# Kernel optimization log

Hardware: AMD Instinct MI355X
Metric: run time of the kernel (lower is better)

## Reference

```python
import jax, jax.numpy as jnp
import numpy as np

N_HEADS = 12
D_MODEL = 768
D_HEAD = 64
LN_EPS = 1e-5


def setup_inputs() -> dict:
    key = jax.random.key(0)
    ks = jax.random.split(key, 7)
    bs, slen = 1, 4096
    s_in = 1.0 / np.sqrt(D_MODEL)
    s_out = 1.0 / np.sqrt(N_HEADS * D_HEAD)
    return {
        "x": jax.random.normal(ks[0], (bs, slen, D_MODEL), jnp.float32),
        "W_attn": jax.random.uniform(ks[1], (D_MODEL, 3 * N_HEADS * D_HEAD), jnp.float32, -s_in, s_in),
        "b_attn": jax.random.uniform(ks[2], (3 * N_HEADS * D_HEAD,), jnp.float32, -s_in, s_in),
        "W_out": jax.random.uniform(ks[3], (N_HEADS * D_HEAD, D_MODEL), jnp.float32, -s_out, s_out),
        "b_out": jax.random.uniform(ks[4], (D_MODEL,), jnp.float32, -s_out, s_out),
        "ln_g": jnp.ones((D_MODEL,), jnp.float32),
        "ln_b": jnp.zeros((D_MODEL,), jnp.float32),
    }


def reference(x, W_attn, b_attn, W_out, b_out, ln_g, ln_b):
    bs, slen, _ = x.shape
    qkv = x @ W_attn + b_attn                      # [b, s, 3*H*D]
    wq, wk, wv = jnp.split(qkv, 3, axis=-1)
    def to_heads(t):
        return t.reshape(bs, slen, N_HEADS, D_HEAD)
    q, k, v = to_heads(wq), to_heads(wk), to_heads(wv)
    # scores: [b, h, s_q, s_k]
    scores = jnp.einsum('bqhd,bkhd->bhqk', q, k) / np.sqrt(D_HEAD).astype(np.float32)
    probs = jax.nn.softmax(scores, axis=-1)
    attn = jnp.einsum('bhqk,bkhd->bqhd', probs, v).reshape(bs, slen, N_HEADS * D_HEAD)
    out = attn @ W_out + b_out
    y = x + out
    mu = jnp.mean(y, axis=-1, keepdims=True)
    var = jnp.mean(jnp.square(y - mu), axis=-1, keepdims=True)
    return (y - mu) / jnp.sqrt(var + LN_EPS) * ln_g + ln_b
```

## Files before the change

### kernel.cpp

```cpp
#include <hip/hip_runtime.h>
#include <cstdint>
#include <cstddef>

#define SL 4096
#define DM 768

typedef short s16x8 __attribute__((ext_vector_type(8)));
typedef unsigned short u16x8 __attribute__((ext_vector_type(8)));
typedef unsigned short u16x4 __attribute__((ext_vector_type(4)));
typedef float f32x4 __attribute__((ext_vector_type(4)));
typedef float f32x16 __attribute__((ext_vector_type(16)));
typedef unsigned int u32x4 __attribute__((ext_vector_type(4)));

__device__ __forceinline__ unsigned short f2bf(float f) {
  unsigned u = __float_as_uint(f);
  u = u + 0x7fffu + ((u >> 16) & 1u);
  return (unsigned short)(u >> 16);
}

__device__ __forceinline__ int swz(int row, int col) {
  return (row << 6) + ((((col >> 3) ^ row) & 7) << 3) + (col & 7);
}

#define ASYNC16(G, L)                                                        \
  __builtin_amdgcn_global_load_lds(                                          \
      (const __attribute__((address_space(1))) void*)(G),                    \
      (__attribute__((address_space(3))) void*)(L), 16, 0, 0)

#define WAITB()                                   \
  do {                                            \
    asm volatile("s_waitcnt vmcnt(0)" ::: "memory"); \
    __builtin_amdgcn_s_barrier();                 \
  } while (0)

#define MF32(A, B, C) __builtin_amdgcn_mfma_f32_32x32x16_bf16((A), (B), (C), 0, 0, 0)

__device__ __forceinline__ void tr_body(
    const float* __restrict__ in, unsigned short* __restrict__ out,
    int R, int C, int bx, int by, float (*tile)[65], int t) {
  const int r0 = by * 64, c0 = bx * 64;
  const int lr = t >> 2, lcb = (t & 3) * 16;
  #pragma unroll
  for (int j = 0; j < 16; j += 4) {
    f32x4 v = *reinterpret_cast<const f32x4*>(in + (size_t)(r0 + lr) * C + c0 + lcb + j);
    tile[lr][lcb + j + 0] = v[0];
    tile[lr][lcb + j + 1] = v[1];
    tile[lr][lcb + j + 2] = v[2];
    tile[lr][lcb + j + 3] = v[3];
  }
  __syncthreads();
  #pragma unroll
  for (int j = 0; j < 16; j += 4) {
    u16x4 o;
    o[0] = f2bf(tile[lcb + j + 0][lr]);
    o[1] = f2bf(tile[lcb + j + 1][lr]);
    o[2] = f2bf(tile[lcb + j + 2][lr]);
    o[3] = f2bf(tile[lcb + j + 3][lr]);
    *reinterpret_cast<u16x4*>(out + (size_t)(c0 + lr) * R + r0 + lcb + j) = o;
  }
}

extern "C" __global__ __launch_bounds__(256) void k_prep(
    const float* __restrict__ x, const float* __restrict__ Wa,
    const float* __restrict__ Wo, unsigned short* __restrict__ xbf,
    unsigned short* __restrict__ wat, unsigned short* __restrict__ wot,
    unsigned* __restrict__ kmx) {
  __shared__ float tile[64][65];
  const int b = blockIdx.x, t = threadIdx.x;
  if (b < 3072) {
    if (b == 0 && t < 12) kmx[t] = 0u;
    const int i = (b * 256 + t) * 4;
    f32x4 v = *reinterpret_cast<const f32x4*>(x + i);
    u16x4 o;
    o[0] = f2bf(v[0]); o[1] = f2bf(v[1]); o[2] = f2bf(v[2]); o[3] = f2bf(v[3]);
    *reinterpret_cast<u16x4*>(xbf + i) = o;
  } else if (b < 3504) {
    const int bb = b - 3072;
    tr_body(Wa, wat, 768, 2304, bb % 36, bb / 36, tile, t);
  } else {
    const int bb = b - 3504;
    tr_body(Wo, wot, 768, 768, bb % 12, bb / 12, tile, t);
  }
}

extern "C" __global__ __launch_bounds__(256) void k_qkv(
    const unsigned short* __restrict__ xbf, const unsigned short* __restrict__ wt,
    const float* __restrict__ bias, unsigned short* __restrict__ qb,
    unsigned short* __restrict__ kbo, unsigned short* __restrict__ vtb,
    float* __restrict__ qn2, unsigned* __restrict__ kmx) {
  __shared__ alignas(16) unsigned short a_lds[2][8192];
  __shared__ alignas(16) unsigned short b_lds[2][8192];
  const int t = threadIdx.x, w = t >> 6, l = t & 63;
  const int l15 = l & 15, lg = l >> 4;
  const int wr = w >> 1, wc = w & 1;
  const int n0 = blockIdx.x * 128, m0 = blockIdx.y * 128;
  f32x4 acc[4][4];
  #pragma unroll
  for (int mt = 0; mt < 4; mt++)
    #pragma unroll
    for (int nt = 0; nt < 4; nt++) acc[mt][nt] = (f32x4)0.f;
  int soff[4];
  #pragma unroll
  for (int c = 0; c < 4; c++) {
    int i = c * 256 + t;
    int row = i >> 3, bp = i & 7;
    soff[c] = row * DM + (bp ^ (row & 7)) * 8;
  }
  const unsigned short* asrc = xbf + (size_t)m0 * DM;
  const unsigned short* bsrc = wt + (size_t)n0 * DM;

#define STAGE128(B, KK)                                                   \
  do {                                                                    \
    _Pragma("unroll")                                                     \
    for (int c = 0; c < 4; c++) {                                         \
      ASYNC16(asrc + (KK) + soff[c], &a_lds[B][0] + c * 2048 + w * 512);  \
      ASYNC16(bsrc + (KK) + soff[c], &b_lds[B][0] + c * 2048 + w * 512);  \
    }                                                                     \
  } while (0)

#define GEMM128(B)                                                            \
  do {                                                                        \
    _Pragma("unroll")                                                         \
    for (int kc = 0; kc < 2; kc++) {                                          \
      s16x8 af[4], bfv[4];                                                    \
      _Pragma("unroll")                                                       \
      for (int mt = 0; mt < 4; mt++)                                          \
        af[mt] = *reinterpret_cast<const s16x8*>(                             \
            &a_lds[B][swz(wr * 64 + mt * 16 + l15, kc * 32 + lg * 8)]);       \
      _Pragma("unroll")                                                       \
      for (int nt = 0; nt < 4; nt++)                                          \
        bfv[nt] = *reinterpret_cast<const s16x8*>(                            \
            &b_lds[B][swz(wc * 64 + nt * 16 + l15, kc * 32 + lg * 8)]);       \
      _Pragma("unroll")                                                       \
      for (int mt = 0; mt < 4; mt++)                                          \
        _Pragma("unroll")                                                     \
        for (int nt = 0; nt < 4; nt++)                                        \
          acc[mt][nt] = __builtin_amdgcn_mfma_f32_16x16x32_bf16(              \
              af[mt], bfv[nt], acc[mt][nt], 0, 0, 0);                         \
    }                                                                         \
  } while (0)

  STAGE128(0, 0);
  WAITB();
  #pragma unroll 1
  for (int kk = 0; kk < DM; kk += 128) {
    STAGE128(1, kk + 64);
    GEMM128(0);
    WAITB();
    if (kk + 128 < DM) STAGE128(0, kk + 128);
    GEMM128(1);
    WAITB();
  }
#undef STAGE128
#undef GEMM128

  const int secn = (n0 >= 1536) ? 2 : (n0 >= 768 ? 1 : 0);
  const int nbase = n0 - secn * 768 + wc * 64;
  const int h = nbase >> 6;
  const int mrow0 = m0 + wr * 64;
  float bv4[4];
  #pragma unroll
  for (int nt = 0; nt < 4; nt++) bv4[nt] = bias[secn * 768 + nbase + nt * 16 + l15];

  if (secn == 0) {
    const float QS = 0.180336880f;
    float s2[4][4];
    #pragma unroll
    for (int mt = 0; mt < 4; mt++) {
      #pragma unroll
      for (int r = 0; r < 4; r++) s2[mt][r] = 0.f;
    }
    #pragma unroll
    for (int mt = 0; mt < 4; mt++) {
      #pragma unroll
      for (int nt = 0; nt < 4; nt++) {
        const int d = nt * 16 + l15;
        #pragma unroll
        for (int r = 0; r < 4; r++) {
          const int m = mrow0 + mt * 16 + lg * 4 + r;
          float v = (acc[mt][nt][r] + bv4[nt]) * QS;
          qb[((size_t)h * SL + m) * 64 + d] = f2bf(v);
          s2[mt][r] = fmaf(v, v, s2[mt][r]);
        }
      }
    }
    #pragma unroll
    for (int mt = 0; mt < 4; mt++)
      #pragma unroll
      for (int r = 0; r < 4; r++) {
        #pragma unroll
        for (int off = 1; off < 16; off <<= 1)
          s2[mt][r] += __shfl_xor(s2[mt][r], off, 64);
      }
    if (l15 == 0) {
      #pragma unroll
      for (int mt = 0; mt < 4; mt++)
        #pragma unroll
        for (int r = 0; r < 4; r++)
          qn2[(size_t)h * SL + mrow0 + mt * 16 + lg * 4 + r] = s2[mt][r];
    }
  } else if (secn == 1) {
    float s2[4][4];
    #pragma unroll
    for (int mt = 0; mt < 4; mt++) {
      #pragma unroll
      for (int r = 0; r < 4; r++) s2[mt][r] = 0.f;
    }
    #pragma unroll
    for (int mt = 0; mt < 4; mt++) {
      #pragma unroll
      for (int nt = 0; nt < 4; nt++) {
        const int d = nt * 16 + l15;
        #pragma unroll
        for (int r = 0; r < 4; r++) {
          const int m = mrow0 + mt * 16 + lg * 4 + r;
          float v = acc[mt][nt][r] + bv4[nt];
          kbo[((size_t)h * SL + m) * 64 + d] = f2bf(v);
          s2[mt][r] = fmaf(v, v, s2[mt][r]);
        }
      }
    }
    float rm = 0.f;
    #pragma unroll
    for (int mt = 0; mt < 4; mt++)
      #pragma unroll
      for (int r = 0; r < 4; r++) {
        #pragma unroll
        for (int off = 1; off < 16; off <<= 1)
          s2[mt][r] += __shfl_xor(s2[mt][r], off, 64);
        rm = fmaxf(rm, s2[mt][r]);
      }
    rm = fmaxf(rm, __shfl_xor(rm, 16, 64));
    rm = fmaxf(rm, __shfl_xor(rm, 32, 64));
    if (l == 0) atomicMax(kmx + h, __float_as_uint(rm));
  } else {
    #pragma unroll
    for (int mt = 0; mt < 4; mt++) {
      #pragma unroll
      for (int nt = 0; nt < 4; nt++) {
        const int d = nt * 16 + l15;
        u16x4 o;
        #pragma unroll
        for (int r = 0; r < 4; r++) o[r] = f2bf(acc[mt][nt][r] + bv4[nt]);
        *reinterpret_cast<u16x4*>(
            vtb + ((size_t)h * 64 + d) * SL + mrow0 + mt * 16 + lg * 4) = o;
      }
    }
  }
}

__device__ __forceinline__ void attn_body32f(
    const unsigned short* kb, const unsigned short* vb,
    const s16x8* qf, f32x16* ot, f32x16& lacc, s16x8 qm,
    const int* kfo, const int* vfo, s16x8 ones) {
  f32x16 st = (f32x16)0.f;
  __builtin_amdgcn_s_setprio(1);
  #pragma unroll
  for (int c = 0; c < 4; c++) {
    s16x8 kf = *reinterpret_cast<const s16x8*>(&kb[kfo[c]]);
    st = MF32(kf, qf[c], st);
  }
  st = MF32(ones, qm, st);
  __builtin_amdgcn_s_setprio(0);
  #pragma unroll
  for (int r = 0; r < 16; r++) st[r] = exp2f(st[r]);
  #pragma unroll
  for (int m = 0; m < 2; m++) {
    const int m0 = m * 8;
    unsigned w0, w1, w2, w3;
    asm("v_cvt_pk_bf16_f32 %0, %1, %2" : "=v"(w0) : "v"(st[m0 + 0]), "v"(st[m0 + 1]));
    asm("v_cvt_pk_bf16_f32 %0, %1, %2" : "=v"(w1) : "v"(st[m0 + 2]), "v"(st[m0 + 3]));
    asm("v_cvt_pk_bf16_f32 %0, %1, %2" : "=v"(w2) : "v"(st[m0 + 4]), "v"(st[m0 + 5]));
    asm("v_cvt_pk_bf16_f32 %0, %1, %2" : "=v"(w3) : "v"(st[m0 + 6]), "v"(st[m0 + 7]));
    asm volatile("v_permlane32_swap_b32 %0, %1" : "+v"(w0), "+v"(w2));
    asm volatile("v_permlane32_swap_b32 %0, %1" : "+v"(w1), "+v"(w3));
    u32x4 wv_;
    wv_[0] = w0; wv_[1] = w1; wv_[2] = w2; wv_[3] = w3;
    s16x8 pbf = *reinterpret_cast<s16x8*>(&wv_);
    __builtin_amdgcn_s_setprio(1);
    #pragma unroll
    for (int dt = 0; dt < 2; dt++) {
      s16x8 vf = *reinterpret_cast<const s16x8*>(&vb[vfo[m * 2 + dt]]);
      ot[dt] = MF32(vf, pbf, ot[dt]);
    }
    lacc = MF32(ones, pbf, lacc);
    __builtin_amdgcn_s_setprio(0);
  }
}

extern "C" __global__ __launch_bounds__(256) void k_attn(
    const unsigned short* __restrict__ qb, const unsigned short* __restrict__ kbi,
    const unsigned short* __restrict__ vt, const float* __restrict__ qn2,
    const unsigned* __restrict__ kmx, unsigned short* __restrict__ aout) {
  __shared__ alignas(16) unsigned char smem[32768];
  unsigned short* kst = (unsigned short*)smem;
  unsigned short* vst = (unsigned short*)(smem + 16384);
  const int t = threadIdx.x, w = t >> 6, l = t & 63;
  const int l31 = l & 31, s = l >> 5;
  const int half = w >> 1, qs = w & 1;
  const int bid = blockIdx.x;
  const int sid = (bid & 7) * 96 + (bid >> 3);
  const int h = sid >> 6, qt = sid & 63;
  const unsigned short* qh = qb + (size_t)h * SL * 64;
  const unsigned short* kh = kbi + ((size_t)h * SL + half * 2048) * 64;
  const unsigned short* vh = vt + (size_t)h * 64 * SL + half * 2048;
  const int q = qt * 64 + qs * 32 + l31;
  const float M = sqrtf(qn2[(size_t)h * SL + q] * __uint_as_float(kmx[h]));
  s16x8 qf[4];
  #pragma unroll
  for (int c = 0; c < 4; c++)
    qf[c] = *reinterpret_cast<const s16x8*>(qh + (size_t)q * 64 + c * 16 + s * 8);
  s16x8 ones;
  #pragma unroll
  for (int e = 0; e < 8; e++) ones[e] = (short)0x3F80;
  s16x8 qm = (s16x8)0;
  if (s == 0) qm[0] = (short)f2bf(-M);
  f32x16 ot[2];
  ot[0] = (f32x16)0.f;
  ot[1] = (f32x16)0.f;
  f32x16 lacc = (f32x16)0.f;
  int koff[2], voff[2];
  #pragma unroll
  for (int c = 0; c < 2; c++) {
    int i = (qs * 2 + c) * 64 + l;
    int row = i >> 3, sb = i & 7;
    int bp = sb ^ ((row ^ (row >> 3)) & 7);
    koff[c] = row * 64 + bp * 8;
    int d = row + 32 * (bp >> 2);
    voff[c] = d * SL + (bp & 3) * 8;
  }
  const int sr = (l31 ^ (l31 >> 3)) & 7;
  int kfo[4], vfo[4];
  #pragma unroll
  for (int c = 0; c < 4; c++) kfo[c] = (l31 << 6) + (((c * 2 + s) ^ sr) << 3);
  #pragma unroll
  for (int m = 0; m < 2; m++)
    #pragma unroll
    for (int dt = 0; dt < 2; dt++)
      vfo[m * 2 + dt] = (l31 << 6) + (((dt * 4 + m * 2 + s) ^ sr) << 3);

#define STAGE_KV(B, LB)                                                     \
  do {                                                                      \
    _Pragma("unroll")                                                       \
    for (int c = 0; c < 2; c++) {                                           \
      ASYNC16(kh + (size_t)(LB) * 64 + koff[c],                             \
              kst + (half * 2 + (B)) * 2048 + (qs * 2 + c) * 512);          \
      ASYNC16(vh + (LB) + voff[c],                                          \
              vst + (half * 2 + (B)) * 2048 + (qs * 2 + c) * 512);          \
    }                                                                       \
  } while (0)

  STAGE_KV(0, 0);
  #pragma unroll 1
  for (int lb = 0; lb < 2048; lb += 64) {
    STAGE_KV(1, lb + 32);
    asm volatile("s_waitcnt vmcnt(4)" ::: "memory");
    __builtin_amdgcn_s_barrier();
    attn_body32f(kst + (half * 2) * 2048, vst + (half * 2) * 2048,
                 qf, ot, lacc, qm, kfo, vfo, ones);
    if (lb + 64 < 2048) {
      STAGE_KV(0, lb + 64);
      asm volatile("s_waitcnt vmcnt(4)" ::: "memory");
    } else {
      asm volatile("s_waitcnt vmcnt(0)" ::: "memory");
    }
    __builtin_amdgcn_s_barrier();
    attn_body32f(kst + (half * 2 + 1) * 2048, vst + (half * 2 + 1) * 2048,
                 qf, ot, lacc, qm, kfo, vfo, ones);
  }
#undef STAGE_KV
  const float lsum = lacc[0];
  float* o_m = (float*)smem;
  float* l_m = (float*)(smem + 17408);
  __syncthreads();
  if (half == 1) {
    #pragma unroll
    for (int dt = 0; dt < 2; dt++) {
      #pragma unroll
      for (int rq = 0; rq < 4; rq++) {
        f32x4 v;
        #pragma unroll
        for (int j = 0; j < 4; j++) v[j] = ot[dt][rq * 4 + j];
        *reinterpret_cast<f32x4*>(&o_m[(qs * 32 + l31) * 68 + dt * 32 + rq * 8 + s * 4]) = v;
      }
    }
    if (s == 0) l_m[qs * 32 + l31] = lsum;
  }
  __syncthreads();
  if (half == 0) {
    const float linv = 1.f / (lsum + l_m[qs * 32 + l31]);
    #pragma unroll
    for (int dt = 0; dt < 2; dt++) {
      #pragma unroll
      for (int rq = 0; rq < 4; rq++) {
        f32x4 vb_ = *reinterpret_cast<const f32x4*>(&o_m[(qs * 32 + l31) * 68 + dt * 32 + rq * 8 + s * 4]);
        u16x4 o;
        #pragma unroll
        for (int j = 0; j < 4; j++)
          o[j] = f2bf((ot[dt][rq * 4 + j] + vb_[j]) * linv);
        *reinterpret_cast<u16x4*>(aout + (size_t)q * DM + h * 64 + dt * 32 + rq * 8 + s * 4) = o;
      }
    }
  }
}

extern "C" __global__ __launch_bounds__(256) void k_out(
    const unsigned short* __restrict__ abf, const unsigned short* __restrict__ wot,
    const float* __restrict__ bias, const float* __restrict__ x, float* __restrict__ y) {
  __shared__ alignas(16) unsigned short a_lds[2][8192];
  __shared__ alignas(16) unsigned short b_lds[2][8192];
  const int t = threadIdx.x, w = t >> 6, l = t & 63;
  const int l15 = l & 15, lg = l >> 4;
  const int wr = w >> 1, wc = w & 1;
  const int n0 = blockIdx.x * 128, m0 = blockIdx.y * 128;
  f32x4 acc[4][4];
  #pragma unroll
  for (int mt = 0; mt < 4; mt++)
    #pragma unroll
    for (int nt = 0; nt < 4; nt++) acc[mt][nt] = (f32x4)0.f;
  int soff[4];
  #pragma unroll
  for (int c = 0; c < 4; c++) {
    int i = c * 256 + t;
    int row = i >> 3, bp = i & 7;
    soff[c] = row * DM + (bp ^ (row & 7)) * 8;
  }
  const unsigned short* asrc = abf + (size_t)m0 * DM;
  const unsigned short* bsrc = wot + (size_t)n0 * DM;

#define STAGE128(B, KK)                                                   \
  do {                                                                    \
    _Pragma("unroll")                                                     \
    for (int c = 0; c < 4; c++) {                                         \
      ASYNC16(asrc + (KK) + soff[c], &a_lds[B][0] + c * 2048 + w * 512);  \
      ASYNC16(bsrc + (KK) + soff[c], &b_lds[B][0] + c * 2048 + w * 512);  \
    }                                                                     \
  } while (0)

#define GEMM128(B)                                                            \
  do {                                                                        \
    _Pragma("unroll")                                                         \
    for (int kc = 0; kc < 2; kc++) {                                          \
      s16x8 af[4], bfv[4];                                                    \
      _Pragma("unroll")                                                       \
      for (int mt = 0; mt < 4; mt++)                                          \
        af[mt] = *reinterpret_cast<const s16x8*>(                             \
            &a_lds[B][swz(wr * 64 + mt * 16 + l15, kc * 32 + lg * 8)]);       \
      _Pragma("unroll")                                                       \
      for (int nt = 0; nt < 4; nt++)                                          \
        bfv[nt] = *reinterpret_cast<const s16x8*>(                            \
            &b_lds[B][swz(wc * 64 + nt * 16 + l15, kc * 32 + lg * 8)]);       \
      _Pragma("unroll")                                                       \
      for (int mt = 0; mt < 4; mt++)                                          \
        _Pragma("unroll")                                                     \
        for (int nt = 0; nt < 4; nt++)                                        \
          acc[mt][nt] = __builtin_amdgcn_mfma_f32_16x16x32_bf16(              \
              af[mt], bfv[nt], acc[mt][nt], 0, 0, 0);                         \
    }                                                                         \
  } while (0)

  STAGE128(0, 0);
  WAITB();
  #pragma unroll 1
  for (int kk = 0; kk < DM; kk += 128) {
    STAGE128(1, kk + 64);
    GEMM128(0);
    WAITB();
    if (kk + 128 < DM) STAGE128(0, kk + 128);
    GEMM128(1);
    WAITB();
  }
#undef STAGE128
#undef GEMM128

  const int mrow0 = m0 + wr * 64;
  #pragma unroll
  for (int nt = 0; nt < 4; nt++) {
    const int n = n0 + wc * 64 + nt * 16 + l15;
    const float bv = bias[n];
    #pragma unroll
    for (int mt = 0; mt < 4; mt++) {
      #pragma unroll
      for (int r = 0; r < 4; r++) {
        const int m = mrow0 + mt * 16 + lg * 4 + r;
        y[(size_t)m * DM + n] = acc[mt][nt][r] + bv + x[(size_t)m * DM + n];
      }
    }
  }
}

extern "C" __global__ __launch_bounds__(256) void k_ln(
    const float* __restrict__ y, const float* __restrict__ g, const float* __restrict__ b,
    float* __restrict__ out) {
  const int row = blockIdx.x, t = threadIdx.x;
  const float* yr = y + (size_t)row * DM;
  float v0 = yr[t], v1 = yr[t + 256], v2 = yr[t + 512];
  float sum = v0 + v1 + v2;
  float sq = v0 * v0 + v1 * v1 + v2 * v2;
  #pragma unroll
  for (int off = 1; off < 64; off <<= 1) {
    sum += __shfl_xor(sum, off, 64);
    sq += __shfl_xor(sq, off, 64);
  }
  __shared__ float ls[8];
  const int wv = t >> 6, l = t & 63;
  if (l == 0) { ls[wv] = sum; ls[4 + wv] = sq; }
  __syncthreads();
  sum = ls[0] + ls[1] + ls[2] + ls[3];
  sq = ls[4] + ls[5] + ls[6] + ls[7];
  const float mu = sum * (1.f / DM);
  const float rstd = rsqrtf(sq * (1.f / DM) - mu * mu + 1e-5f);
  out[(size_t)row * DM + t] = (v0 - mu) * rstd * g[t] + b[t];
  out[(size_t)row * DM + t + 256] = (v1 - mu) * rstd * g[t + 256] + b[t + 256];
  out[(size_t)row * DM + t + 512] = (v2 - mu) * rstd * g[t + 512] + b[t + 512];
}

extern "C" void kernel_launch(void* const* d_in, const int* in_sizes, int n_in,
                              void* d_out, int out_size, void* d_ws, size_t ws_size,
                              hipStream_t stream) {
  (void)in_sizes; (void)n_in; (void)out_size; (void)ws_size;
  const float* x = (const float*)d_in[0];
  const float* Wa = (const float*)d_in[1];
  const float* ba = (const float*)d_in[2];
  const float* Wo = (const float*)d_in[3];
  const float* bo = (const float*)d_in[4];
  const float* lng = (const float*)d_in[5];
  const float* lnb = (const float*)d_in[6];
  float* out = (float*)d_out;

  unsigned short* ws16 = (unsigned short*)d_ws;
  unsigned short* xbf = ws16;
  unsigned short* wat = xbf + 3145728;
  unsigned short* wot = wat + 1769472;
  unsigned short* qbf = wot + 589824;
  unsigned short* kbf = qbf + 3145728;
  unsigned short* vtb = kbf + 3145728;
  unsigned short* aob = vtb + 3145728;
  float* ybuf = (float*)(aob + 3145728);
  float* qn2 = ybuf + 3145728;
  unsigned* kmx = (unsigned*)(qn2 + 49152);

  k_prep<<<3648, 256, 0, stream>>>(x, Wa, Wo, xbf, wat, wot, kmx);
  k_qkv<<<dim3(18, 32), 256, 0, stream>>>(xbf, wat, ba, qbf, kbf, vtb, qn2, kmx);
  k_attn<<<768, 256, 0, stream>>>(qbf, kbf, vtb, qn2, kmx, aob);
  k_out<<<dim3(6, 32), 256, 0, stream>>>(aob, wot, bo, x, ybuf);
  k_ln<<<4096, 256, 0, stream>>>(ybuf, lng, lnb, out);
}
```

Before: 168.5 us.

## Software-pipeline attention loop: overlap QK MFMAs with previous tile's PV and exp

Restructures the attention inner loop into a three-buffer rotating pipeline. The QK^T MFMAs for tile n are interleaved with the PV MFMAs of tile n-1, and the exp/bf16 packing for tile n runs after the async K/V prefetch for tile n+2 is issued. The goal is to hide exp and conversion latency behind matrix-core work and to deepen prefetch. In exchange it uses more shared memory (48KB instead of 32KB), which can lower occupancy, and it keeps extra registers live for the packed probabilities.

Result: slower. 172.6 us (+2.4%).

```diff
diff --git a/kernel.cpp b/kernel.cpp
--- a/kernel.cpp
+++ b/kernel.cpp
@@ -249,52 +249,11 @@
   }
 }
 
-__device__ __forceinline__ void attn_body32f(
-    const unsigned short* kb, const unsigned short* vb,
-    const s16x8* qf, f32x16* ot, f32x16& lacc, s16x8 qm,
-    const int* kfo, const int* vfo, s16x8 ones) {
-  f32x16 st = (f32x16)0.f;
-  __builtin_amdgcn_s_setprio(1);
-  #pragma unroll
-  for (int c = 0; c < 4; c++) {
-    s16x8 kf = *reinterpret_cast<const s16x8*>(&kb[kfo[c]]);
-    st = MF32(kf, qf[c], st);
-  }
-  st = MF32(ones, qm, st);
-  __builtin_amdgcn_s_setprio(0);
-  #pragma unroll
-  for (int r = 0; r < 16; r++) st[r] = exp2f(st[r]);
-  #pragma unroll
-  for (int m = 0; m < 2; m++) {
-    const int m0 = m * 8;
-    unsigned w0, w1, w2, w3;
-    asm("v_cvt_pk_bf16_f32 %0, %1, %2" : "=v"(w0) : "v"(st[m0 + 0]), "v"(st[m0 + 1]));
-    asm("v_cvt_pk_bf16_f32 %0, %1, %2" : "=v"(w1) : "v"(st[m0 + 2]), "v"(st[m0 + 3]));
-    asm("v_cvt_pk_bf16_f32 %0, %1, %2" : "=v"(w2) : "v"(st[m0 + 4]), "v"(st[m0 + 5]));
-    asm("v_cvt_pk_bf16_f32 %0, %1, %2" : "=v"(w3) : "v"(st[m0 + 6]), "v"(st[m0 + 7]));
-    asm volatile("v_permlane32_swap_b32 %0, %1" : "+v"(w0), "+v"(w2));
-    asm volatile("v_permlane32_swap_b32 %0, %1" : "+v"(w1), "+v"(w3));
-    u32x4 wv_;
-    wv_[0] = w0; wv_[1] = w1; wv_[2] = w2; wv_[3] = w3;
-    s16x8 pbf = *reinterpret_cast<s16x8*>(&wv_);
-    __builtin_amdgcn_s_setprio(1);
-    #pragma unroll
-    for (int dt = 0; dt < 2; dt++) {
-      s16x8 vf = *reinterpret_cast<const s16x8*>(&vb[vfo[m * 2 + dt]]);
-      ot[dt] = MF32(vf, pbf, ot[dt]);
-    }
-    lacc = MF32(ones, pbf, lacc);
-    __builtin_amdgcn_s_setprio(0);
-  }
-}
-
 extern "C" __global__ __launch_bounds__(256) void k_attn(
     const unsigned short* __restrict__ qb, const unsigned short* __restrict__ kbi,
     const unsigned short* __restrict__ vt, const float* __restrict__ qn2,
     const unsigned* __restrict__ kmx, unsigned short* __restrict__ aout) {
-  __shared__ alignas(16) unsigned char smem[32768];
-  unsigned short* kst = (unsigned short*)smem;
-  unsigned short* vst = (unsigned short*)(smem + 16384);
+  __shared__ alignas(16) unsigned char smem[49152];
   const int t = threadIdx.x, w = t >> 6, l = t & 63;
   const int l31 = l & 31, s = l >> 5;
   const int half = w >> 1, qs = w & 1;
@@ -319,6 +278,7 @@
   ot[0] = (f32x16)0.f;
   ot[1] = (f32x16)0.f;
   f32x16 lacc = (f32x16)0.f;
+  s16x8 pb0, pb1;
   int koff[2], voff[2];
   #pragma unroll
   for (int c = 0; c < 2; c++) {
@@ -338,37 +298,114 @@
     #pragma unroll
     for (int dt = 0; dt < 2; dt++)
       vfo[m * 2 + dt] = (l31 << 6) + (((dt * 4 + m * 2 + s) ^ sr) << 3);
-
-#define STAGE_KV(B, LB)                                                     \
+  unsigned short* hb = (unsigned short*)smem + half * 12288;
+  unsigned short* p0 = hb;
+  unsigned short* p1 = hb + 4096;
+  unsigned short* p2 = hb + 8192;
+
+#define STAGE_T(DP, TT)                                                   \
+  do {                                                                    \
+    _Pragma("unroll")                                                     \
+    for (int c = 0; c < 2; c++) {                                         \
+      ASYNC16(kh + (size_t)(TT) * 32 * 64 + koff[c], (DP) + (qs * 2 + c) * 512); \
+      ASYNC16(vh + (TT) * 32 + voff[c], (DP) + 2048 + (qs * 2 + c) * 512);       \
+    }                                                                     \
+  } while (0)
+
+#define LDF(P, O) (*reinterpret_cast<const s16x8*>((P) + (O)))
+
+#define EXPPACK(ST)                                                              \
+  do {                                                                           \
+    _Pragma("unroll")                                                            \
+    for (int r = 0; r < 16; r++) ST[r] = exp2f(ST[r]);                           \
+    unsigned w0, w1, w2, w3;                                                     \
+    asm("v_cvt_pk_bf16_f32 %0, %1, %2" : "=v"(w0) : "v"(ST[0]), "v"(ST[1]));     \
+    asm("v_cvt_pk_bf16_f32 %0, %1, %2" : "=v"(w1) : "v"(ST[2]), "v"(ST[3]));     \
+    asm("v_cvt_pk_bf16_f32 %0, %1, %2" : "=v"(w2) : "v"(ST[4]), "v"(ST[5]));     \
+    asm("v_cvt_pk_bf16_f32 %0, %1, %2" : "=v"(w3) : "v"(ST[6]), "v"(ST[7]));     \
+    asm volatile("v_permlane32_swap_b32 %0, %1" : "+v"(w0), "+v"(w2));           \
+    asm volatile("v_permlane32_swap_b32 %0, %1" : "+v"(w1), "+v"(w3));           \
+    u32x4 wa_;                                                                   \
+    wa_[0] = w0; wa_[1] = w1; wa_[2] = w2; wa_[3] = w3;                          \
+    pb0 = *reinterpret_cast<s16x8*>(&wa_);                                       \
+    asm("v_cvt_pk_bf16_f32 %0, %1, %2" : "=v"(w0) : "v"(ST[8]), "v"(ST[9]));     \
+    asm("v_cvt_pk_bf16_f32 %0, %1, %2" : "=v"(w1) : "v"(ST[10]), "v"(ST[11]));   \
+    asm("v_cvt_pk_bf16_f32 %0, %1, %2" : "=v"(w2) : "v"(ST[12]), "v"(ST[13]));   \
+    asm("v_cvt_pk_bf16_f32 %0, %1, %2" : "=v"(w3) : "v"(ST[14]), "v"(ST[15]));   \
+    asm volatile("v_permlane32_swap_b32 %0, %1" : "+v"(w0), "+v"(w2));           \
+    asm volatile("v_permlane32_swap_b32 %0, %1" : "+v"(w1), "+v"(w3));           \
+    u32x4 wb_;                                                                   \
+    wb_[0] = w0; wb_[1] = w1; wb_[2] = w2; wb_[3] = w3;                          \
+    pb1 = *reinterpret_cast<s16x8*>(&wb_);                                       \
+  } while (0)
+
+#define PIPE_BODY(PK, PVS, NN)                                              \
   do {                                                                      \
-    _Pragma("unroll")                                                       \
-    for (int c = 0; c < 2; c++) {                                           \
-      ASYNC16(kh + (size_t)(LB) * 64 + koff[c],                             \
-              kst + (half * 2 + (B)) * 2048 + (qs * 2 + c) * 512);          \
-      ASYNC16(vh + (LB) + voff[c],                                          \
-              vst + (half * 2 + (B)) * 2048 + (qs * 2 + c) * 512);          \
+    f32x16 st = (f32x16)0.f;                                                \
+    __builtin_amdgcn_s_setprio(1);                                          \
+    st = MF32(LDF(PK, kfo[0]), qf[0], st);                                  \
+    ot[0] = MF32(LDF((PVS) + 2048, vfo[0]), pb0, ot[0]);                    \
+    st = MF32(LDF(PK, kfo[1]), qf[1], st);                                  \
+    ot[1] = MF32(LDF((PVS) + 2048, vfo[1]), pb0, ot[1]);                    \
+    st = MF32(LDF(PK, kfo[2]), qf[2], st);                                  \
+    lacc = MF32(ones, pb0, lacc);                                           \
+    st = MF32(LDF(PK, kfo[3]), qf[3], st);                                  \
+    ot[0] = MF32(LDF((PVS) + 2048, vfo[2]), pb1, ot[0]);                    \
+    st = MF32(ones, qm, st);                                                \
+    ot[1] = MF32(LDF((PVS) + 2048, vfo[3]), pb1, ot[1]);                    \
+    lacc = MF32(ones, pb1, lacc);                                           \
+    __builtin_amdgcn_s_setprio(0);                                          \
+    if ((NN) + 2 < 64) {                                                    \
+      STAGE_T(PVS, (NN) + 2);                                               \
+      EXPPACK(st);                                                          \
+      asm volatile("s_waitcnt vmcnt(4)" ::: "memory");                      \
+    } else {                                                                \
+      EXPPACK(st);                                                          \
+      asm volatile("s_waitcnt vmcnt(0)" ::: "memory");                      \
     }                                                                       \
-  } while (0)
-
-  STAGE_KV(0, 0);
-  #pragma unroll 1
-  for (int lb = 0; lb < 2048; lb += 64) {
-    STAGE_KV(1, lb + 32);
+    __builtin_amdgcn_s_barrier();                                           \
+  } while (0)
+
+  STAGE_T(p0, 0);
+  STAGE_T(p1, 1);
+  asm volatile("s_waitcnt vmcnt(4)" ::: "memory");
+  __builtin_amdgcn_s_barrier();
+  {
+    f32x16 st = (f32x16)0.f;
+    __builtin_amdgcn_s_setprio(1);
+    st = MF32(LDF(p0, kfo[0]), qf[0], st);
+    st = MF32(LDF(p0, kfo[1]), qf[1], st);
+    st = MF32(LDF(p0, kfo[2]), qf[2], st);
+    st = MF32(LDF(p0, kfo[3]), qf[3], st);
+    st = MF32(ones, qm, st);
+    __builtin_amdgcn_s_setprio(0);
+    STAGE_T(p2, 2);
+    EXPPACK(st);
     asm volatile("s_waitcnt vmcnt(4)" ::: "memory");
     __builtin_amdgcn_s_barrier();
-    attn_body32f(kst + (half * 2) * 2048, vst + (half * 2) * 2048,
-                 qf, ot, lacc, qm, kfo, vfo, ones);
-    if (lb + 64 < 2048) {
-      STAGE_KV(0, lb + 64);
-      asm volatile("s_waitcnt vmcnt(4)" ::: "memory");
-    } else {
-      asm volatile("s_waitcnt vmcnt(0)" ::: "memory");
-    }
-    __builtin_amdgcn_s_barrier();
-    attn_body32f(kst + (half * 2 + 1) * 2048, vst + (half * 2 + 1) * 2048,
-                 qf, ot, lacc, qm, kfo, vfo, ones);
-  }
-#undef STAGE_KV
+  }
+  #pragma unroll 1
+  for (int it = 0; it < 21; ++it) {
+    const int n = 1 + it * 3;
+    PIPE_BODY(p1, p0, n);
+    PIPE_BODY(p2, p1, n + 1);
+    PIPE_BODY(p0, p2, n + 2);
+  }
+  {
+    __builtin_amdgcn_s_setprio(1);
+    ot[0] = MF32(LDF(p0 + 2048, vfo[0]), pb0, ot[0]);
+    ot[1] = MF32(LDF(p0 + 2048, vfo[1]), pb0, ot[1]);
+    lacc = MF32(ones, pb0, lacc);
+    ot[0] = MF32(LDF(p0 + 2048, vfo[2]), pb1, ot[0]);
+    ot[1] = MF32(LDF(p0 + 2048, vfo[3]), pb1, ot[1]);
+    lacc = MF32(ones, pb1, lacc);
+    __builtin_amdgcn_s_setprio(0);
+  }
+#undef PIPE_BODY
+#undef EXPPACK
+#undef STAGE_T
+#undef LDF
+
   const float lsum = lacc[0];
   float* o_m = (float*)smem;
   float* l_m = (float*)(smem + 17408);
```

## Split attention KV range across two blocks and add a combine kernel

Applied to the files above, without the earlier changes.

The attention kernel now launches twice as many blocks, each covering half the key range, with its two wave groups splitting that half further. Unnormalized partial outputs (bf16) and row sums go to a workspace, and a new k_norm kernel adds the two partials and normalizes. This raises parallelism across the 256 CUs, since 768 blocks underfill the machine. In exchange it adds a kernel launch, extra global traffic for the partials, and an extra bf16 rounding on the unnormalized partials. This works only because a fixed max bound is used, so no rescaling is needed when combining.

Measured after the change: 172.9 us. 2.6% more time.

```diff
diff --git a/kernel.cpp b/kernel.cpp
--- a/kernel.cpp
+++ b/kernel.cpp
@@ -16,6 +16,9 @@
   unsigned u = __float_as_uint(f);
   u = u + 0x7fffu + ((u >> 16) & 1u);
   return (unsigned short)(u >> 16);
+}
+__device__ __forceinline__ float bf2f(unsigned short v) {
+  return __uint_as_float((unsigned)v << 16);
 }
 
 __device__ __forceinline__ int swz(int row, int col) {
@@ -291,19 +294,23 @@
 extern "C" __global__ __launch_bounds__(256) void k_attn(
     const unsigned short* __restrict__ qb, const unsigned short* __restrict__ kbi,
     const unsigned short* __restrict__ vt, const float* __restrict__ qn2,
-    const unsigned* __restrict__ kmx, unsigned short* __restrict__ aout) {
+    const unsigned* __restrict__ kmx, unsigned short* __restrict__ obuf,
+    float* __restrict__ lbuf) {
   __shared__ alignas(16) unsigned char smem[32768];
   unsigned short* kst = (unsigned short*)smem;
   unsigned short* vst = (unsigned short*)(smem + 16384);
   const int t = threadIdx.x, w = t >> 6, l = t & 63;
   const int l31 = l & 31, s = l >> 5;
-  const int half = w >> 1, qs = w & 1;
+  const int sub = w >> 1, qs = w & 1;
   const int bid = blockIdx.x;
-  const int sid = (bid & 7) * 96 + (bid >> 3);
-  const int h = sid >> 6, qt = sid & 63;
+  const int sid = (bid & 7) * 192 + (bid >> 3);
+  const int h = sid >> 7;
+  const int rem = sid & 127;
+  const int qt = rem >> 1, half = rem & 1;
   const unsigned short* qh = qb + (size_t)h * SL * 64;
-  const unsigned short* kh = kbi + ((size_t)h * SL + half * 2048) * 64;
-  const unsigned short* vh = vt + (size_t)h * 64 * SL + half * 2048;
+  const int kvbase = half * 2048 + sub * 1024;
+  const unsigned short* kh = kbi + ((size_t)h * SL + kvbase) * 64;
+  const unsigned short* vh = vt + (size_t)h * 64 * SL + kvbase;
   const int q = qt * 64 + qs * 32 + l31;
   const float M = sqrtf(qn2[(size_t)h * SL + q] * __uint_as_float(kmx[h]));
   s16x8 qf[4];
@@ -344,28 +351,28 @@
     _Pragma("unroll")                                                       \
     for (int c = 0; c < 2; c++) {                                           \
       ASYNC16(kh + (size_t)(LB) * 64 + koff[c],                             \
-              kst + (half * 2 + (B)) * 2048 + (qs * 2 + c) * 512);          \
+              kst + (sub * 2 + (B)) * 2048 + (qs * 2 + c) * 512);           \
       ASYNC16(vh + (LB) + voff[c],                                          \
-              vst + (half * 2 + (B)) * 2048 + (qs * 2 + c) * 512);          \
+              vst + (sub * 2 + (B)) * 2048 + (qs * 2 + c) * 512);           \
     }                                                                       \
   } while (0)
 
   STAGE_KV(0, 0);
   #pragma unroll 1
-  for (int lb = 0; lb < 2048; lb += 64) {
+  for (int lb = 0; lb < 1024; lb += 64) {
     STAGE_KV(1, lb + 32);
     asm volatile("s_waitcnt vmcnt(4)" ::: "memory");
     __builtin_amdgcn_s_barrier();
-    attn_body32f(kst + (half * 2) * 2048, vst + (half * 2) * 2048,
+    attn_body32f(kst + (sub * 2) * 2048, vst + (sub * 2) * 2048,
                  qf, ot, lacc, qm, kfo, vfo, ones);
-    if (lb + 64 < 2048) {
+    if (lb + 64 < 1024) {
       STAGE_KV(0, lb + 64);
       asm volatile("s_waitcnt vmcnt(4)" ::: "memory");
     } else {
       asm volatile("s_waitcnt vmcnt(0)" ::: "memory");
     }
     __builtin_amdgcn_s_barrier();
-    attn_body32f(kst + (half * 2 + 1) * 2048, vst + (half * 2 + 1) * 2048,
+    attn_body32f(kst + (sub * 2 + 1) * 2048, vst + (sub * 2 + 1) * 2048,
                  qf, ot, lacc, qm, kfo, vfo, ones);
   }
 #undef STAGE_KV
@@ -373,7 +380,7 @@
   float* o_m = (float*)smem;
   float* l_m = (float*)(smem + 17408);
   __syncthreads();
-  if (half == 1) {
+  if (sub == 1) {
     #pragma unroll
     for (int dt = 0; dt < 2; dt++) {
       #pragma unroll
@@ -387,8 +394,9 @@
     if (s == 0) l_m[qs * 32 + l31] = lsum;
   }
   __syncthreads();
-  if (half == 0) {
-    const float linv = 1.f / (lsum + l_m[qs * 32 + l31]);
+  if (sub == 0) {
+    const float ltot = lsum + l_m[qs * 32 + l31];
+    unsigned short* od = obuf + (size_t)half * SL * DM;
     #pragma unroll
     for (int dt = 0; dt < 2; dt++) {
       #pragma unroll
@@ -397,11 +405,27 @@
         u16x4 o;
         #pragma unroll
         for (int j = 0; j < 4; j++)
-          o[j] = f2bf((ot[dt][rq * 4 + j] + vb_[j]) * linv);
-        *reinterpret_cast<u16x4*>(aout + (size_t)q * DM + h * 64 + dt * 32 + rq * 8 + s * 4) = o;
-      }
-    }
-  }
+          o[j] = f2bf(ot[dt][rq * 4 + j] + vb_[j]);
+        *reinterpret_cast<u16x4*>(od + (size_t)q * DM + h * 64 + dt * 32 + rq * 8 + s * 4) = o;
+      }
+    }
+    if (s == 0) lbuf[half * 49152 + h * SL + q] = ltot;
+  }
+}
+
+extern "C" __global__ __launch_bounds__(256) void k_norm(
+    const unsigned short* __restrict__ obuf, const float* __restrict__ lbuf,
+    unsigned short* __restrict__ aob) {
+  const int idx = blockIdx.x * 256 + threadIdx.x;
+  const int row = idx / 192, c4 = idx % 192;
+  const int h = c4 >> 4;
+  const float li = 1.f / (lbuf[h * SL + row] + lbuf[49152 + h * SL + row]);
+  u16x4 a = *reinterpret_cast<const u16x4*>(obuf + (size_t)idx * 4);
+  u16x4 b = *reinterpret_cast<const u16x4*>(obuf + (size_t)SL * DM + (size_t)idx * 4);
+  u16x4 o;
+  #pragma unroll
+  for (int j = 0; j < 4; j++) o[j] = f2bf((bf2f(a[j]) + bf2f(b[j])) * li);
+  *reinterpret_cast<u16x4*>(aob + (size_t)idx * 4) = o;
 }
 
 extern "C" __global__ __launch_bounds__(256) void k_out(
@@ -539,10 +563,13 @@
   float* ybuf = (float*)(aob + 3145728);
   float* qn2 = ybuf + 3145728;
   unsigned* kmx = (unsigned*)(qn2 + 49152);
+  float* lbuf = (float*)(kmx + 16);
+  unsigned short* obuf = (unsigned short*)(lbuf + 98304);
 
   k_prep<<<3648, 256, 0, stream>>>(x, Wa, Wo, xbf, wat, wot, kmx);
   k_qkv<<<dim3(18, 32), 256, 0, stream>>>(xbf, wat, ba, qbf, kbf, vtb, qn2, kmx);
-  k_attn<<<768, 256, 0, stream>>>(qbf, kbf, vtb, qn2, kmx, aob);
+  k_attn<<<1536, 256, 0, stream>>>(qbf, kbf, vtb, qn2, kmx, obuf, lbuf);
+  k_norm<<<3072, 256, 0, stream>>>(obuf, lbuf, aob);
   k_out<<<dim3(6, 32), 256, 0, stream>>>(aob, wot, bo, x, ybuf);
   k_ln<<<4096, 256, 0, stream>>>(ybuf, lng, lnb, out);
 }
```
